# Kernel tuning notes

Hardware: AMD Instinct MI355X
Metric: run time of the kernel (lower is better)

The kernel has to match this reference:

```python
import jax, jax.numpy as jnp
import numpy as np

B, S, D, H = 64, 256, 2048, 16
HD = D // H  # 128
MAXS = 256


def setup_inputs() -> dict:
    key = jax.random.key(0)
    ks = jax.random.split(key, 16)
    sc = 0.02
    inp = {
        "q": jax.random.normal(ks[0], (B, S, D), jnp.float32),
        "k": jax.random.normal(ks[1], (B, S, D), jnp.float32),
        "v": jax.random.normal(ks[2], (B, S, D), jnp.float32),
        "attention_mask": jax.random.randint(ks[3], (B, S), 0, 2, jnp.int32),
        # projection weights, torch Linear convention: y = x @ W.T + b
        "Wq": jax.random.normal(ks[4], (D, D), jnp.float32) * sc,
        "bq": jnp.zeros((D,), jnp.float32),
        "Wk": jax.random.normal(ks[5], (D, D), jnp.float32) * sc,
        "bk": jnp.zeros((D,), jnp.float32),
        "Wv": jax.random.normal(ks[6], (D, D), jnp.float32) * sc,
        "bv": jnp.zeros((D,), jnp.float32),
        "Wo": jax.random.normal(ks[7], (D, D), jnp.float32) * sc,
        "bo": jnp.zeros((D,), jnp.float32),
        # additive per-head bias table (max_sequence_length=256)
        "bias_table": jax.random.normal(ks[8], (H, MAXS, MAXS), jnp.float32) * 0.1,
    }
    return inp


def reference(q, k, v, attention_mask, Wq, bq, Wk, bk, Wv, bv, Wo, bo, bias_table):
    def proj(x, W, b):  # (B,S,D) -> (B,H,S,HD)
        y = x @ W.T + b
        return y.reshape(B, S, H, HD).transpose(0, 2, 1, 3)

    qh = proj(q, Wq, bq)
    kh = proj(k, Wk, bk)
    vh = proj(v, Wv, bv)

    # (B,H,Sq,Sk) scores
    scores = jnp.einsum("bhqd,bhkd->bhqk", qh, kh) / jnp.sqrt(jnp.float32(HD))
    scores = scores + bias_table[None, :, :S, :S]
    # mask: (B,Sk) -> (B,1,1,Sk); masked_fill where mask==0
    neg_inf = jnp.finfo(scores.dtype).min
    scores = jnp.where(attention_mask[:, None, None, :] == 0, neg_inf, scores)
    probs = jax.nn.softmax(scores, axis=-1)  # dropout p=0.0 -> identity
    out = jnp.einsum("bhqk,bhkd->bhqd", probs, vh)
    out = out.transpose(0, 2, 1, 3).reshape(B, S, D)
    return out @ Wo.T + bo
```

## Files before the change

### kernel.cpp

```cpp
#include <hip/hip_runtime.h>
#include <hip/hip_bf16.h>

typedef __attribute__((ext_vector_type(4))) float f32x4;
typedef __attribute__((ext_vector_type(8))) short s16x8;
typedef __attribute__((ext_vector_type(4))) unsigned short u16x4;
typedef __attribute__((ext_vector_type(8))) unsigned short u16x8;
typedef __attribute__((ext_vector_type(4))) int i32x4;

#define NB 64
#define NS 256
#define ND 2048
#define NH 16
#define NHD 128

__device__ __forceinline__ unsigned short f2bf(float f){
  unsigned int u = __float_as_uint(f);
  u += 0x7fffu + ((u >> 16) & 1u);
  return (unsigned short)(u >> 16);
}

__device__ __forceinline__ void gload16(const void* g, void* l){
  __builtin_amdgcn_global_load_lds(
    (const __attribute__((address_space(1))) unsigned int*)g,
    (__attribute__((address_space(3))) unsigned int*)l, 16, 0, 0);
}

#define SBAR()  __builtin_amdgcn_sched_barrier(0)
#define BARRIER() do{ SBAR(); __builtin_amdgcn_s_barrier(); SBAR(); }while(0)
#define WAIT_LGKM0() do{ asm volatile("s_waitcnt lgkmcnt(0)" ::: "memory"); SBAR(); }while(0)
#define WAIT_VM0()   do{ asm volatile("s_waitcnt vmcnt(0)"   ::: "memory"); SBAR(); }while(0)
#define WAIT_VM8()   do{ asm volatile("s_waitcnt vmcnt(8)"   ::: "memory"); SBAR(); }while(0)

__global__ __launch_bounds__(256) void wconv(const float* __restrict__ s,
                                             unsigned short* __restrict__ d, int n8){
  int i = blockIdx.x*256 + threadIdx.x;
  if (i >= n8) return;
  f32x4 a = *(const f32x4*)(s + (size_t)i*8);
  f32x4 b = *(const f32x4*)(s + (size_t)i*8 + 4);
  u16x8 u;
  #pragma unroll
  for (int r=0;r<4;r++){ u[r]=f2bf(a[r]); u[4+r]=f2bf(b[r]); }
  *(u16x8*)(d + (size_t)i*8) = u;
}

template<int OUTMODE>
__global__ __launch_bounds__(512, 2) void gemm256(
    const unsigned short* __restrict__ A, const unsigned short* __restrict__ Bw,
    const float* __restrict__ bias, void* __restrict__ Out, int m_base)
{
  extern __shared__ __attribute__((aligned(16))) char ldsb[];
  const int tid  = threadIdx.x;
  const int lane = tid & 63, wid = tid >> 6;
  const int g = lane >> 4, l15 = lane & 15;
  const int wm = wid >> 2, wn = wid & 3;

  const int nwg = gridDim.x, bid = blockIdx.x;
  const int swz = (bid & 7) * (nwg >> 3) + (bid >> 3);
  const int mt = swz >> 3, nt = swz & 7;
  const int m0 = mt*256, n0 = nt*256;

  const int srow_l = tid >> 3;
  const int scol   = (((tid & 7) ^ (srow_l & 7)) * 8);
  const unsigned short* gsrc[4];
  gsrc[0] = A  + (size_t)(m0 +       srow_l)*ND + scol;
  gsrc[1] = A  + (size_t)(m0 + 128 + srow_l)*ND + scol;
  gsrc[2] = Bw + (size_t)(n0 +       srow_l)*ND + scol;
  gsrc[3] = Bw + (size_t)(n0 + 128 + srow_l)*ND + scol;

#define STAGE(buf, p, kt) do{ \
    const unsigned short* s_ = gsrc[p] + (kt); \
    char* d_ = ldsb + (buf)*65536 + ((p)>>1)*32768 + ((p)&1)*16384 + tid*16; \
    gload16(s_, d_); gload16(s_ + (size_t)64*ND, d_ + 8192); }while(0)

#define RD_A(buf, qa) do{ \
    _Pragma("unroll") for (int i_=0;i_<4;i_++){ \
      int hr = (qa)*64 + i_*16 + l15; \
      const char* p_ = ldsb + (buf)*65536 + wm*16384 + hr*128; \
      _Pragma("unroll") for (int ks_=0;ks_<2;ks_++) \
        av[i_][ks_] = *(const s16x8*)(p_ + (((ks_*4+g) ^ (hr&7))*16)); } }while(0)

#define RD_B(buf, dst, qb) do{ \
    _Pragma("unroll") for (int j_=0;j_<2;j_++){ \
      int hc = (wn&1)*64 + (qb)*32 + j_*16 + l15; \
      const char* p_ = ldsb + (buf)*65536 + 32768 + (wn>>1)*16384 + hc*128; \
      _Pragma("unroll") for (int ks_=0;ks_<2;ks_++) \
        dst[j_][ks_] = *(const s16x8*)(p_ + (((ks_*4+g) ^ (hc&7))*16)); } }while(0)

#define MFMA_PH(qa, qb, bv) do{ \
    __builtin_amdgcn_s_setprio(1); \
    _Pragma("unroll") for (int i_=0;i_<4;i_++) \
      _Pragma("unroll") for (int j_=0;j_<2;j_++) \
        _Pragma("unroll") for (int ks_=0;ks_<2;ks_++) \
          acc[(qa)*4+i_][(qb)*2+j_] = __builtin_amdgcn_mfma_f32_16x16x32_bf16( \
              av[i_][ks_], bv[j_][ks_], acc[(qa)*4+i_][(qb)*2+j_], 0,0,0); \
    __builtin_amdgcn_s_setprio(0); }while(0)

#define HALF(buf, kt_next, doStage) do{ \
    RD_A(buf,0); RD_B(buf,bva,0); \
    BARRIER(); WAIT_LGKM0(); \
    MFMA_PH(0,0,bva); \
    BARRIER(); \
    RD_B(buf,bvb,1); \
    BARRIER(); WAIT_LGKM0(); \
    MFMA_PH(0,1,bvb); \
    BARRIER(); \
    RD_A(buf,1); \
    WAIT_LGKM0(); BARRIER(); \
    if ((doStage)==1){ STAGE(buf,0,kt_next); STAGE(buf,1,kt_next); \
                       STAGE(buf,2,kt_next); STAGE(buf,3,kt_next); } \
    MFMA_PH(1,0,bva); \
    MFMA_PH(1,1,bvb); \
    if ((doStage)==1){ WAIT_VM8(); BARRIER(); } \
    else if ((doStage)==2){ WAIT_VM0(); BARRIER(); } \
  }while(0)

  f32x4 acc[8][4];
  s16x8 av[4][2], bva[2][2], bvb[2][2];

  STAGE(0,0,0); STAGE(0,1,0); STAGE(0,2,0); STAGE(0,3,0);
  STAGE(1,0,64); STAGE(1,1,64); STAGE(1,2,64); STAGE(1,3,64);
  #pragma unroll
  for (int i=0;i<8;i++)
    #pragma unroll
    for (int j=0;j<4;j++) acc[i][j] = f32x4{0.f,0.f,0.f,0.f};
  WAIT_VM8();
  BARRIER();

  for (int t = 0; t < 15; ++t) {
    HALF(0, (2*t+2)*64, 1);
    HALF(1, (2*t+3)*64, 1);
  }
  HALF(0, 0, 2);
  HALF(1, 0, 3);

  #pragma unroll
  for (int jx=0;jx<4;jx++){
    int n = n0 + wn*64 + ((jx>>1)<<5) + ((jx&1)<<4) + l15;
    float bj = bias[n];
    #pragma unroll
    for (int i=0;i<8;i++){
      int mb = m_base + m0 + wm*128 + ((i>>2)<<6) + ((i&3)<<4) + g*4;
      if (OUTMODE == 2){
        float* O = (float*)Out;
        #pragma unroll
        for (int r=0;r<4;r++) O[(size_t)(mb+r)*ND + n] = acc[i][jx][r] + bj;
      } else if (OUTMODE == 0){
        unsigned short* O = (unsigned short*)Out;
        int bb = mb >> 8, h = n >> 7, d = n & 127, s0 = mb & 255;
        #pragma unroll
        for (int r=0;r<4;r++)
          O[(((size_t)bb*NH + h)*NS + s0 + r)*NHD + d] = f2bf(acc[i][jx][r] + bj);
      } else {
        unsigned short* O = (unsigned short*)Out;
        int bb = mb >> 8, h = n >> 7, d = n & 127, s0 = mb & 255;
        u16x4 u;
        #pragma unroll
        for (int r=0;r<4;r++) u[r] = f2bf(acc[i][jx][r] + bj);
        *(u16x4*)(O + (((size_t)bb*NH + h)*NHD + d)*NS + s0) = u;
      }
    }
  }
#undef STAGE
#undef RD_A
#undef RD_B
#undef MFMA_PH
#undef HALF
}

__global__ __launch_bounds__(512, 1) void attn_fused2(
  const unsigned short* __restrict__ Qh, const unsigned short* __restrict__ Kh,
  const unsigned short* __restrict__ VT, const int* __restrict__ mask,
  const float* __restrict__ bias_table, unsigned short* __restrict__ AO)
{
  __shared__ unsigned short Klds[256*128];
  __shared__ unsigned short Vlds[128*256];
  char* Kb_ = (char*)Klds; char* Vb_ = (char*)Vlds;
  const int bh = blockIdx.x, b = bh >> 4, h = bh & 15;
  const int tid = threadIdx.x, lane = tid & 63, w = tid >> 6;
  const int g = lane >> 4, l15 = lane & 15;

  {
    const unsigned short* Ksrc = Kh + (size_t)bh*NS*NHD;
    int r0 = tid >> 4, sl = tid & 15;
    #pragma unroll
    for (int c=0;c<8;c++){
      int row = c*32 + r0;
      gload16(Ksrc + (size_t)row*NHD + ((sl ^ (row&7))*8), Kb_ + c*8192 + tid*16);
    }
  }
  {
    const unsigned short* Vsrc = VT + (size_t)bh*NHD*NS;
    int r0 = tid >> 5, sl = tid & 31;
    #pragma unroll
    for (int c=0;c<8;c++){
      int row = c*16 + r0;
      gload16(Vsrc + (size_t)row*NS + ((sl ^ (row&7))*8), Vb_ + c*8192 + tid*16);
    }
  }
  WAIT_VM8();
  BARRIER();

  const float scale = 0.08838834764831845f;
  const int* mrow = mask + b*NS;
  const int s0l = l15 + ((g&1)<<5), s1l = s0l + 16;
  const int sel = g >> 1;

  auto pass = [&](int p, bool wait_v){
    const int q = w*32 + p*16 + l15;
    const unsigned short* Qrow = Qh + ((size_t)bh*NS + q)*NHD;
    s16x8 bq[4];
    #pragma unroll
    for (int kk=0;kk<4;kk++) bq[kk] = *(const s16x8*)(Qrow + kk*32 + g*8);

    f32x4 c[16];
    __builtin_amdgcn_s_setprio(1);
    #pragma unroll
    for (int kb=0;kb<16;kb++){
      c[kb] = f32x4{0.f,0.f,0.f,0.f};
      int row = kb*16 + l15;
      #pragma unroll
      for (int kk=0;kk<4;kk++){
        s16x8 a = *(const s16x8*)(Kb_ + row*256 + (((kk*4+g) ^ (row&7))*16));
        c[kb] = __builtin_amdgcn_mfma_f32_16x16x32_bf16(a, bq[kk], c[kb], 0,0,0);
      }
    }
    __builtin_amdgcn_s_setprio(0);

    const float* brow = bias_table + ((size_t)h*NS + q)*NS;
    float mx = -3.0e38f;
    #pragma unroll
    for (int kb=0;kb<16;kb++){
      f32x4 b4 = *(const f32x4*)(brow + kb*16 + g*4);
      i32x4 m4 = *(const i32x4*)(mrow + kb*16 + g*4);
      #pragma unroll
      for (int r=0;r<4;r++){
        float val = (m4[r] != 0) ? (c[kb][r]*scale + b4[r]) : -3.0e38f;
        c[kb][r] = val;
        mx = fmaxf(mx, val);
      }
    }
    mx = fmaxf(mx, __shfl_xor(mx, 16));
    mx = fmaxf(mx, __shfl_xor(mx, 32));
    float sum = 0.f;
    #pragma unroll
    for (int kb=0;kb<16;kb++)
      #pragma unroll
      for (int r=0;r<4;r++){
        float pv = __expf(c[kb][r] - mx);
        c[kb][r] = pv; sum += pv;
      }
    sum += __shfl_xor(sum, 16);
    sum += __shfl_xor(sum, 32);
    float inv = 1.f / sum;

    unsigned int pk[16][2];
    #pragma unroll
    for (int kb=0;kb<16;kb++){
      pk[kb][0] = (unsigned int)f2bf(c[kb][0]*inv) | ((unsigned int)f2bf(c[kb][1]*inv) << 16);
      pk[kb][1] = (unsigned int)f2bf(c[kb][2]*inv) | ((unsigned int)f2bf(c[kb][3]*inv) << 16);
    }

    if (wait_v){ WAIT_VM0(); BARRIER(); }

    s16x8 pb[8];
    #pragma unroll
    for (int kk=0;kk<8;kk++){
      unsigned int e0 = (unsigned int)__shfl((int)pk[2*kk][0],   s0l);
      unsigned int e1 = (unsigned int)__shfl((int)pk[2*kk][1],   s0l);
      unsigned int e2 = (unsigned int)__shfl((int)pk[2*kk][0],   s1l);
      unsigned int e3 = (unsigned int)__shfl((int)pk[2*kk][1],   s1l);
      unsigned int o0 = (unsigned int)__shfl((int)pk[2*kk+1][0], s0l);
      unsigned int o1 = (unsigned int)__shfl((int)pk[2*kk+1][1], s0l);
      unsigned int o2 = (unsigned int)__shfl((int)pk[2*kk+1][0], s1l);
      unsigned int o3 = (unsigned int)__shfl((int)pk[2*kk+1][1], s1l);
      union { unsigned int wd[4]; s16x8 v; } u_;
      u_.wd[0] = sel ? o0 : e0; u_.wd[1] = sel ? o1 : e1;
      u_.wd[2] = sel ? o2 : e2; u_.wd[3] = sel ? o3 : e3;
      pb[kk] = u_.v;
    }

    f32x4 oacc[8];
    __builtin_amdgcn_s_setprio(1);
    #pragma unroll
    for (int dt=0;dt<8;dt++){
      oacc[dt] = f32x4{0.f,0.f,0.f,0.f};
      int row = dt*16 + l15;
      #pragma unroll
      for (int kk=0;kk<8;kk++){
        s16x8 a = *(const s16x8*)(Vb_ + row*512 + (((kk*4+g) ^ (row&7))*16));
        oacc[dt] = __builtin_amdgcn_mfma_f32_16x16x32_bf16(a, pb[kk], oacc[dt], 0,0,0);
      }
    }
    __builtin_amdgcn_s_setprio(0);

    #pragma unroll
    for (int dt=0;dt<8;dt++){
      u16x4 u;
      #pragma unroll
      for (int r=0;r<4;r++) u[r] = f2bf(oacc[dt][r]);
      *(u16x4*)(AO + ((size_t)b*NS + q)*ND + h*NHD + dt*16 + g*4) = u;
    }
  };

  pass(0, true);
  pass(1, false);
}

extern "C" void kernel_launch(void* const* d_in, const int* in_sizes, int n_in,
                              void* d_out, int out_size, void* d_ws, size_t ws_size,
                              hipStream_t stream)
{
  const float* q  = (const float*)d_in[0];
  const float* k  = (const float*)d_in[1];
  const float* v  = (const float*)d_in[2];
  const int* mask = (const int*)d_in[3];
  const float* Wq = (const float*)d_in[4];
  const float* bq = (const float*)d_in[5];
  const float* Wk = (const float*)d_in[6];
  const float* bk = (const float*)d_in[7];
  const float* Wv = (const float*)d_in[8];
  const float* bv = (const float*)d_in[9];
  const float* Wo = (const float*)d_in[10];
  const float* bo = (const float*)d_in[11];
  const float* bias_table = (const float*)d_in[12];

  char* ws = (char*)d_ws;
  unsigned short* Wob = (unsigned short*)(ws + 0);
  unsigned short* wb  = (unsigned short*)(ws + 8388608);
  unsigned short* tmp = (unsigned short*)(ws + 16777216);
  unsigned short* Qh  = (unsigned short*)(ws + 83886080);
  unsigned short* Kh  = (unsigned short*)(ws + 150994944);
  unsigned short* VT  = (unsigned short*)(ws + 218103808);
  unsigned short* AO  = (unsigned short*)(ws + 285212672);

  hipFuncSetAttribute((const void*)gemm256<0>, hipFuncAttributeMaxDynamicSharedMemorySize, 131072);
  hipFuncSetAttribute((const void*)gemm256<1>, hipFuncAttributeMaxDynamicSharedMemorySize, 131072);
  hipFuncSetAttribute((const void*)gemm256<2>, hipFuncAttributeMaxDynamicSharedMemorySize, 131072);

  wconv<<<2048,256,0,stream>>>(Wo, Wob, 524288);

  const float* acts[3]  = {q, k, v};
  const float* wgt[3]   = {Wq, Wk, Wv};
  const float* bia[3]   = {bq, bk, bv};
  unsigned short* outs[3] = {Qh, Kh, VT};

  for (int x = 0; x < 3; ++x) {
    wconv<<<2048,256,0,stream>>>(wgt[x], wb, 524288);
    wconv<<<16384,256,0,stream>>>(acts[x], tmp, 4194304);
    if (x < 2)
      gemm256<0><<<512,512,131072,stream>>>(tmp, wb, bia[x], outs[x], 0);
    else
      gemm256<1><<<512,512,131072,stream>>>(tmp, wb, bia[x], outs[x], 0);
  }

  attn_fused2<<<1024,512,0,stream>>>(Qh,Kh,VT,mask,bias_table,AO);
  gemm256<2><<<512,512,131072,stream>>>(AO,Wob,bo,(float*)d_out,0);
}
```

Measured before the change: 778.3 us.

## Interleave global-to-LDS staging across GEMM phases with split-buffer prefetch

Restructures the GEMM main loop so that global-to-LDS loads for the next K tile are issued in quarters, interleaved between the MFMA phases, instead of all four stages at once after the LDS reads. The A-part of the other buffer is staged early while the current buffer's B-part is refilled later, and the wait tightens from vmcnt(8) to vmcnt(4). The aim is to spread memory traffic and hide load latency behind compute. The trade-off is finer-grained synchronisation and added barriers, with a risk of LDS read/write hazards if the buffer reuse ordering is wrong.

```diff
diff --git a/kernel.cpp b/kernel.cpp
--- a/kernel.cpp
+++ b/kernel.cpp
@@ -29,6 +29,7 @@
 #define BARRIER() do{ SBAR(); __builtin_amdgcn_s_barrier(); SBAR(); }while(0)
 #define WAIT_LGKM0() do{ asm volatile("s_waitcnt lgkmcnt(0)" ::: "memory"); SBAR(); }while(0)
 #define WAIT_VM0()   do{ asm volatile("s_waitcnt vmcnt(0)"   ::: "memory"); SBAR(); }while(0)
+#define WAIT_VM4()   do{ asm volatile("s_waitcnt vmcnt(4)"   ::: "memory"); SBAR(); }while(0)
 #define WAIT_VM8()   do{ asm volatile("s_waitcnt vmcnt(8)"   ::: "memory"); SBAR(); }while(0)
 
 __global__ __launch_bounds__(256) void wconv(const float* __restrict__ s,
@@ -95,43 +96,46 @@
               av[i_][ks_], bv[j_][ks_], acc[(qa)*4+i_][(qb)*2+j_], 0,0,0); \
     __builtin_amdgcn_s_setprio(0); }while(0)
 
-#define HALF(buf, kt_next, doStage) do{ \
-    RD_A(buf,0); RD_B(buf,bva,0); \
+#define HALF(d, ktA, ktB, wmode) do{ \
+    RD_A(d,0); RD_B(d,bva,0); \
+    if ((ktA)>=0) STAGE((d)^1, 0, ktA); \
     BARRIER(); WAIT_LGKM0(); \
     MFMA_PH(0,0,bva); \
     BARRIER(); \
-    RD_B(buf,bvb,1); \
+    RD_B(d,bvb,1); \
+    if ((ktA)>=0) STAGE((d)^1, 1, ktA); \
     BARRIER(); WAIT_LGKM0(); \
     MFMA_PH(0,1,bvb); \
     BARRIER(); \
-    RD_A(buf,1); \
-    WAIT_LGKM0(); BARRIER(); \
-    if ((doStage)==1){ STAGE(buf,0,kt_next); STAGE(buf,1,kt_next); \
-                       STAGE(buf,2,kt_next); STAGE(buf,3,kt_next); } \
+    RD_A(d,1); \
+    if ((ktB)>=0) STAGE(d, 2, ktB); \
+    BARRIER(); WAIT_LGKM0(); \
     MFMA_PH(1,0,bva); \
+    BARRIER(); \
+    if ((ktB)>=0) STAGE(d, 3, ktB); \
     MFMA_PH(1,1,bvb); \
-    if ((doStage)==1){ WAIT_VM8(); BARRIER(); } \
-    else if ((doStage)==2){ WAIT_VM0(); BARRIER(); } \
+    if ((wmode)==0){ WAIT_VM4(); BARRIER(); } \
+    else if ((wmode)==1){ WAIT_VM0(); BARRIER(); } \
   }while(0)
 
   f32x4 acc[8][4];
   s16x8 av[4][2], bva[2][2], bvb[2][2];
 
   STAGE(0,0,0); STAGE(0,1,0); STAGE(0,2,0); STAGE(0,3,0);
-  STAGE(1,0,64); STAGE(1,1,64); STAGE(1,2,64); STAGE(1,3,64);
+  STAGE(1,2,64); STAGE(1,3,64);
   #pragma unroll
   for (int i=0;i<8;i++)
     #pragma unroll
     for (int j=0;j<4;j++) acc[i][j] = f32x4{0.f,0.f,0.f,0.f};
-  WAIT_VM8();
+  WAIT_VM4();
   BARRIER();
 
   for (int t = 0; t < 15; ++t) {
-    HALF(0, (2*t+2)*64, 1);
-    HALF(1, (2*t+3)*64, 1);
-  }
-  HALF(0, 0, 2);
-  HALF(1, 0, 3);
+    HALF(0, (2*t+1)*64, (2*t+2)*64, 0);
+    HALF(1, (2*t+2)*64, (2*t+3)*64, 0);
+  }
+  HALF(0, 31*64, -1, 1);
+  HALF(1, -1, -1, -1);
 
   #pragma unroll
   for (int jx=0;jx<4;jx++){
```

Result: faster. 745.6 us (-4.2%).
